# Kernel optimization log

Measured on AMD Instinct MI355X. Metric: run time of the kernel, lower is better.

## Reference

```python
import jax, jax.numpy as jnp
import numpy as np

N_NODES = 50000
N_EDGES = 800000
IN_DIM, HID_DIM, OUT_DIM = 128, 96, 40


def setup_inputs() -> dict:
    key = jax.random.key(0)
    ks = jax.random.split(key, 8)
    x = jax.random.normal(ks[0], (N_NODES, IN_DIM), dtype=jnp.float32)
    edge_src = jax.random.randint(ks[1], (N_EDGES,), 0, N_NODES, dtype=jnp.int32)
    edge_dst = jax.random.randint(ks[2], (N_EDGES,), 0, N_NODES, dtype=jnp.int32)
    edge_val = jax.random.uniform(ks[3], (N_EDGES,), dtype=jnp.float32)
    W1 = jax.random.normal(ks[4], (IN_DIM, HID_DIM), dtype=jnp.float32) * 0.05
    b1 = jax.random.normal(ks[5], (HID_DIM,), dtype=jnp.float32) * 0.05
    W2 = jax.random.normal(ks[6], (HID_DIM, OUT_DIM), dtype=jnp.float32) * 0.05
    b2 = jax.random.normal(ks[7], (OUT_DIM,), dtype=jnp.float32) * 0.05
    return {"x": x, "edge_val": edge_val, "W1": W1, "b1": b1,
            "W2": W2, "b2": b2, "edge_src": edge_src, "edge_dst": edge_dst}


def _spmm(edge_src, edge_dst, edge_val, dense, num_nodes):
    # out[i] = sum_{e: dst[e]==i} val[e] * dense[src[e]]  (COO sparse @ dense)
    msgs = edge_val[:, None] * dense[edge_src]  # [E, D]
    return jax.ops.segment_sum(msgs, edge_dst, num_segments=num_nodes)


def reference(x, edge_val, W1, b1, W2, b2, edge_src, edge_dst):
    n = x.shape[0]
    # GraphConv 1: support = x @ W1; out = A @ support + b1
    h = _spmm(edge_src, edge_dst, edge_val, x @ W1, n) + b1
    h = jax.nn.relu(h)  # dropout is identity in eval mode
    # GraphConv 2
    out = _spmm(edge_src, edge_dst, edge_val, h @ W2, n) + b2
    return jax.nn.log_softmax(out, axis=1)
```

## Files before the change

kernel.cpp:

```cpp
#include <hip/hip_runtime.h>
#include <hip/hip_fp16.h>
#include <math.h>

#define N_NODES 50000
#define N_EDGES 800000
#define IN_DIM 128
#define HID_DIM 96
#define OUT_DIM 40
#define CAP 48
#define NB_G1 782
#define NB_CHUNK8 391
#define SLICE 6250

typedef __attribute__((ext_vector_type(8))) unsigned short ushort8_t;
typedef __attribute__((ext_vector_type(8))) short short8_t;
typedef __attribute__((ext_vector_type(4))) float floatx4_t;

static __device__ __forceinline__ unsigned short f2bf(float f) {
    unsigned int u = __float_as_uint(f);
    u += 0x7FFFu + ((u >> 16) & 1u);
    return (unsigned short)(u >> 16);
}
static __device__ __forceinline__ float bf2f(unsigned short h) {
    return __uint_as_float(((unsigned int)h) << 16);
}
static __device__ __forceinline__ float rec2w(unsigned int r) {
    return __half2float(__ushort_as_half((unsigned short)(r >> 16)));
}

__global__ __launch_bounds__(256) void gemm1_fill_kernel(
    const float* __restrict__ x, const float* __restrict__ W1,
    unsigned short* __restrict__ supb,
    const int* __restrict__ esrc, const int* __restrict__ edst,
    const float* __restrict__ eval, int* __restrict__ cnt,
    unsigned int* __restrict__ recs, int n) {
    const int b = blockIdx.x;
    const int t = threadIdx.x;

    if (b >= NB_G1) {
        const int i = b - NB_G1;
        const int slice = b & 7;
        const int chunk = i >> 3;
        const int e0 = chunk * 2048 + t * 8;
        if (e0 < N_EDGES) {
            const int4 d4a = *(const int4*)(edst + e0);
            const int4 d4b = *(const int4*)(edst + e0 + 4);
            const int lo = slice * SLICE;
            int dv[8] = {d4a.x, d4a.y, d4a.z, d4a.w,
                         d4b.x, d4b.y, d4b.z, d4b.w};
            #pragma unroll
            for (int j = 0; j < 8; ++j) {
                int d = dv[j];
                if ((unsigned)(d - lo) < (unsigned)SLICE) {
                    int e = e0 + j;
                    int pos = atomicAdd(&cnt[d], 1);
                    if (pos < CAP) {
                        unsigned int rec = (unsigned int)esrc[e] |
                            ((unsigned int)__half_as_ushort(__float2half(eval[e])) << 16);
                        recs[(size_t)d * CAP + pos] = rec;
                    }
                }
            }
        }
        return;
    }

    __shared__ unsigned short sB[24 * 64 * 8];
    for (int i = t; i < IN_DIM * HID_DIM; i += 256) {
        int k = i / HID_DIM, nn = i - k * HID_DIM;
        int c = k >> 5, q = (k >> 3) & 3, j = k & 7;
        int g = nn >> 4, l16 = nn & 15;
        sB[(((c * 6 + g) * 64) + q * 16 + l16) * 8 + j] = f2bf(W1[i]);
    }
    __syncthreads();

    const int wave = t >> 6, lane = t & 63;
    const int m = lane & 15, q = lane >> 4;
    const int r0 = b * 64 + wave * 16;
    const int row = r0 + m;
    const bool rok = row < n;

    floatx4_t acc[6];
    #pragma unroll
    for (int g = 0; g < 6; ++g) acc[g] = (floatx4_t){0.f, 0.f, 0.f, 0.f};

    #pragma unroll
    for (int c = 0; c < 4; ++c) {
        float4 a0 = make_float4(0.f, 0.f, 0.f, 0.f), a1 = a0;
        if (rok) {
            const float4* xp = (const float4*)(x + (size_t)row * IN_DIM + c * 32 + q * 8);
            a0 = xp[0];
            a1 = xp[1];
        }
        short8_t af;
        af[0] = (short)f2bf(a0.x); af[1] = (short)f2bf(a0.y);
        af[2] = (short)f2bf(a0.z); af[3] = (short)f2bf(a0.w);
        af[4] = (short)f2bf(a1.x); af[5] = (short)f2bf(a1.y);
        af[6] = (short)f2bf(a1.z); af[7] = (short)f2bf(a1.w);
        #pragma unroll
        for (int g = 0; g < 6; ++g) {
            short8_t bf = *(const short8_t*)&sB[(((c * 6 + g) * 64) + lane) * 8];
            acc[g] = __builtin_amdgcn_mfma_f32_16x16x32_bf16(af, bf, acc[g], 0, 0, 0);
        }
    }

    #pragma unroll
    for (int r = 0; r < 4; ++r) {
        int ro = r0 + q * 4 + r;
        if (ro < n) {
            #pragma unroll
            for (int g = 0; g < 6; ++g)
                supb[(size_t)ro * HID_DIM + g * 16 + m] = f2bf(acc[g][r]);
        }
    }
}

__global__ __launch_bounds__(256) void gather1_gemm2_kernel(
    const unsigned short* __restrict__ supb, const unsigned int* __restrict__ recs,
    const int* __restrict__ cnt, const float* __restrict__ b1,
    const float* __restrict__ W2, unsigned short* __restrict__ yb) {
    __shared__ float sH[21][HID_DIM + 4];
    __shared__ float sW2[HID_DIM * OUT_DIM];
    __shared__ unsigned int sRec[21][52];
    const int t = threadIdx.x;
    const int dst0 = blockIdx.x * 21;
    const int g = t / 12, l = t % 12;
    const int dst = dst0 + g;
    const bool active = (t < 252) && (dst < N_NODES);

    for (int i = t; i < HID_DIM * OUT_DIM / 4; i += 256)
        ((float4*)sW2)[i] = ((const float4*)W2)[i];

    for (int i = t; i < 21 * 12; i += 256) {
        int gg = i / 12, qq = i % 12;
        int dd = dst0 + gg;
        if (dd < N_NODES)
            ((uint4*)&sRec[gg][0])[qq] = ((const uint4*)(recs + (size_t)dd * CAP))[qq];
    }
    __syncthreads();

    if (active) {
        int deg = cnt[dst];
        deg = deg < CAP ? deg : CAP;
        float acc[8] = {};
        const int c8 = l;
        const unsigned int* rg = &sRec[g][0];
        int p = 0;
        for (; p + 4 <= deg; p += 4) {
            unsigned int r0 = rg[p + 0], r1 = rg[p + 1];
            unsigned int r2 = rg[p + 2], r3 = rg[p + 3];
            ushort8_t v0 = ((const ushort8_t*)(supb + (size_t)(r0 & 0xFFFFu) * HID_DIM))[c8];
            ushort8_t v1 = ((const ushort8_t*)(supb + (size_t)(r1 & 0xFFFFu) * HID_DIM))[c8];
            ushort8_t v2 = ((const ushort8_t*)(supb + (size_t)(r2 & 0xFFFFu) * HID_DIM))[c8];
            ushort8_t v3 = ((const ushort8_t*)(supb + (size_t)(r3 & 0xFFFFu) * HID_DIM))[c8];
            float w0 = rec2w(r0), w1 = rec2w(r1), w2 = rec2w(r2), w3 = rec2w(r3);
            #pragma unroll
            for (int j = 0; j < 8; ++j) {
                acc[j] += w0 * bf2f(v0[j]);
                acc[j] += w1 * bf2f(v1[j]);
                acc[j] += w2 * bf2f(v2[j]);
                acc[j] += w3 * bf2f(v3[j]);
            }
        }
        for (; p < deg; ++p) {
            unsigned int r = rg[p];
            ushort8_t sv = ((const ushort8_t*)(supb + (size_t)(r & 0xFFFFu) * HID_DIM))[c8];
            float v = rec2w(r);
            #pragma unroll
            for (int j = 0; j < 8; ++j) acc[j] += v * bf2f(sv[j]);
        }
        float4 r0, r1;
        r0.x = fmaxf(acc[0] + b1[c8 * 8 + 0], 0.f);
        r0.y = fmaxf(acc[1] + b1[c8 * 8 + 1], 0.f);
        r0.z = fmaxf(acc[2] + b1[c8 * 8 + 2], 0.f);
        r0.w = fmaxf(acc[3] + b1[c8 * 8 + 3], 0.f);
        r1.x = fmaxf(acc[4] + b1[c8 * 8 + 4], 0.f);
        r1.y = fmaxf(acc[5] + b1[c8 * 8 + 5], 0.f);
        r1.z = fmaxf(acc[6] + b1[c8 * 8 + 6], 0.f);
        r1.w = fmaxf(acc[7] + b1[c8 * 8 + 7], 0.f);
        float4* hp = (float4*)&sH[g][c8 * 8];
        hp[0] = r0;
        hp[1] = r1;
    }
    __syncthreads();

    for (int idx = t; idx < 21 * OUT_DIM; idx += 256) {
        int d = idx / OUT_DIM, c = idx % OUT_DIM;
        int dd = dst0 + d;
        if (dd >= N_NODES) continue;
        const float4* hr = (const float4*)&sH[d][0];
        float s = 0.f;
        #pragma unroll
        for (int k4 = 0; k4 < HID_DIM / 4; ++k4) {
            float4 hv = hr[k4];
            s += hv.x * sW2[(k4 * 4 + 0) * OUT_DIM + c]
               + hv.y * sW2[(k4 * 4 + 1) * OUT_DIM + c]
               + hv.z * sW2[(k4 * 4 + 2) * OUT_DIM + c]
               + hv.w * sW2[(k4 * 4 + 3) * OUT_DIM + c];
        }
        yb[(size_t)dd * OUT_DIM + c] = f2bf(s);
    }
}

__global__ __launch_bounds__(256) void gather2_lsm_kernel(
    const unsigned short* __restrict__ yb, const unsigned int* __restrict__ recs,
    const int* __restrict__ cnt, const float* __restrict__ b2,
    float* __restrict__ out) {
    __shared__ unsigned int sRec[50][52];
    __shared__ float part[256];
    __shared__ float smax[50];
    __shared__ float ssum[50];
    const int t = threadIdx.x;
    const int g = t / 5;
    const int c8 = t % 5;
    int dst = blockIdx.x * 50 + g;
    bool active = (t < 250) && (dst < N_NODES);

    for (int i = t; i < 50 * 12; i += 256) {
        int gg = i / 12, qq = i % 12;
        int dd = blockIdx.x * 50 + gg;
        if (dd < N_NODES)
            ((uint4*)&sRec[gg][0])[qq] = ((const uint4*)(recs + (size_t)dd * CAP))[qq];
    }
    __syncthreads();

    float acc[8] = {};
    if (active) {
        int deg = cnt[dst];
        deg = deg < CAP ? deg : CAP;
        const unsigned int* rg = &sRec[g][0];
        int p = 0;
        for (; p + 4 <= deg; p += 4) {
            unsigned int r0 = rg[p + 0], r1 = rg[p + 1];
            unsigned int r2 = rg[p + 2], r3 = rg[p + 3];
            ushort8_t v0 = ((const ushort8_t*)(yb + (size_t)(r0 & 0xFFFFu) * OUT_DIM))[c8];
            ushort8_t v1 = ((const ushort8_t*)(yb + (size_t)(r1 & 0xFFFFu) * OUT_DIM))[c8];
            ushort8_t v2 = ((const ushort8_t*)(yb + (size_t)(r2 & 0xFFFFu) * OUT_DIM))[c8];
            ushort8_t v3 = ((const ushort8_t*)(yb + (size_t)(r3 & 0xFFFFu) * OUT_DIM))[c8];
            float w0 = rec2w(r0), w1 = rec2w(r1), w2 = rec2w(r2), w3 = rec2w(r3);
            #pragma unroll
            for (int j = 0; j < 8; ++j) {
                acc[j] += w0 * bf2f(v0[j]);
                acc[j] += w1 * bf2f(v1[j]);
                acc[j] += w2 * bf2f(v2[j]);
                acc[j] += w3 * bf2f(v3[j]);
            }
        }
        for (; p < deg; ++p) {
            unsigned int r = rg[p];
            ushort8_t sv = ((const ushort8_t*)(yb + (size_t)(r & 0xFFFFu) * OUT_DIM))[c8];
            float v = rec2w(r);
            #pragma unroll
            for (int j = 0; j < 8; ++j) acc[j] += v * bf2f(sv[j]);
        }
        #pragma unroll
        for (int j = 0; j < 8; ++j) acc[j] += b2[c8 * 8 + j];
    }
    float lmax = -INFINITY;
    #pragma unroll
    for (int j = 0; j < 8; ++j) lmax = fmaxf(lmax, acc[j]);
    part[t] = active ? lmax : -INFINITY;
    __syncthreads();
    if (t < 50) {
        float m = part[t * 5];
        #pragma unroll
        for (int i = 1; i < 5; ++i) m = fmaxf(m, part[t * 5 + i]);
        smax[t] = m;
    }
    __syncthreads();
    float m = active ? smax[g] : 0.f;
    float lsum = 0.f;
    #pragma unroll
    for (int j = 0; j < 8; ++j) lsum += expf(acc[j] - m);
    part[t] = active ? lsum : 0.f;
    __syncthreads();
    if (t < 50) {
        float s = 0.f;
        #pragma unroll
        for (int i = 0; i < 5; ++i) s += part[t * 5 + i];
        ssum[t] = logf(s);
    }
    __syncthreads();
    if (active) {
        float ls = ssum[g];
        float* op = out + (size_t)dst * OUT_DIM + c8 * 8;
        ((float4*)op)[0] = make_float4(acc[0] - m - ls, acc[1] - m - ls,
                                       acc[2] - m - ls, acc[3] - m - ls);
        ((float4*)op)[1] = make_float4(acc[4] - m - ls, acc[5] - m - ls,
                                       acc[6] - m - ls, acc[7] - m - ls);
    }
}

extern "C" void kernel_launch(void* const* d_in, const int* in_sizes, int n_in,
                              void* d_out, int out_size, void* d_ws, size_t ws_size,
                              hipStream_t stream) {
    const float* x        = (const float*)d_in[0];
    const float* edge_val = (const float*)d_in[1];
    const float* W1       = (const float*)d_in[2];
    const float* b1       = (const float*)d_in[3];
    const float* W2       = (const float*)d_in[4];
    const float* b2       = (const float*)d_in[5];
    const int*   esrc     = (const int*)d_in[6];
    const int*   edst     = (const int*)d_in[7];
    float* out = (float*)d_out;

    int*   cnt  = (int*)d_ws;
    unsigned int* recs = (unsigned int*)(cnt + 50048);
    unsigned short* supb = (unsigned short*)(recs + (size_t)N_NODES * CAP);
    unsigned short* yb   = supb + (size_t)N_NODES * HID_DIM;

    hipMemsetAsync(cnt, 0, N_NODES * sizeof(int), stream);
    gemm1_fill_kernel<<<NB_G1 + NB_CHUNK8 * 8, 256, 0, stream>>>(
        x, W1, supb, esrc, edst, edge_val, cnt, recs, N_NODES);
    gather1_gemm2_kernel<<<(N_NODES + 20) / 21, 256, 0, stream>>>(
        supb, recs, cnt, b1, W2, yb);
    gather2_lsm_kernel<<<(N_NODES + 49) / 50, 256, 0, stream>>>(
        yb, recs, cnt, b2, out);
}
```

Measured before the change: 183.3 us.

## Fuse three GCN stages into one cooperative kernel with grid syncs

Replaces the three separate launches (gemm1+bucket fill, gather1+gemm2, gather2+log_softmax) with a single persistent cooperative kernel of 1016 blocks that uses grid-wide syncs between phases. Blocks loop over work items in phases that previously had more blocks than the grid. The aim is to remove kernel launch gaps and tail effects between stages. In exchange it adds grid-sync cost, a fixed grid that may underfill some phases, and a fallback to the old path if the cooperative launch fails.

```diff
diff --git a/kernel.cpp b/kernel.cpp
--- a/kernel.cpp
+++ b/kernel.cpp
@@ -1,5 +1,6 @@
 #include <hip/hip_runtime.h>
 #include <hip/hip_fp16.h>
+#include <hip/hip_cooperative_groups.h>
 #include <math.h>
 
 #define N_NODES 50000
@@ -9,12 +10,18 @@
 #define OUT_DIM 40
 #define CAP 48
 #define NB_G1 782
-#define NB_CHUNK8 391
+#define GRID 1016
+#define FILL_PB 127
+#define NCHUNK 391
 #define SLICE 6250
+#define NGRP_B 2381
+#define NGRP_C 1000
 
 typedef __attribute__((ext_vector_type(8))) unsigned short ushort8_t;
 typedef __attribute__((ext_vector_type(8))) short short8_t;
 typedef __attribute__((ext_vector_type(4))) float floatx4_t;
+
+namespace cg = cooperative_groups;
 
 static __device__ __forceinline__ unsigned short f2bf(float f) {
     unsigned int u = __float_as_uint(f);
@@ -26,6 +33,276 @@
 }
 static __device__ __forceinline__ float rec2w(unsigned int r) {
     return __half2float(__ushort_as_half((unsigned short)(r >> 16)));
+}
+
+__global__ __launch_bounds__(256, 4) void fused_kernel(
+    const float* __restrict__ x, const float* __restrict__ W1,
+    unsigned short* __restrict__ supb,
+    const int* __restrict__ esrc, const int* __restrict__ edst,
+    const float* __restrict__ eval, int* __restrict__ cnt,
+    unsigned int* __restrict__ recs,
+    const float* __restrict__ b1, const float* __restrict__ W2,
+    const float* __restrict__ b2,
+    unsigned short* __restrict__ yb, float* __restrict__ out) {
+    __shared__ __align__(16) unsigned char smem[28160];
+    const int bid = blockIdx.x;
+    const int t = threadIdx.x;
+    cg::grid_group gg_grid = cg::this_grid();
+
+    if (bid < NB_G1) {
+        unsigned short* sB = (unsigned short*)smem;
+        for (int i = t; i < IN_DIM * HID_DIM; i += 256) {
+            int k = i / HID_DIM, nn = i - k * HID_DIM;
+            int c = k >> 5, q2 = (k >> 3) & 3, j = k & 7;
+            int g2 = nn >> 4, l16 = nn & 15;
+            sB[(((c * 6 + g2) * 64) + q2 * 16 + l16) * 8 + j] = f2bf(W1[i]);
+        }
+        __syncthreads();
+
+        const int wave = t >> 6, lane = t & 63;
+        const int m = lane & 15, q = lane >> 4;
+        const int r0 = bid * 64 + wave * 16;
+        const int row = r0 + m;
+        const bool rok = row < N_NODES;
+
+        floatx4_t acc[6];
+        #pragma unroll
+        for (int g = 0; g < 6; ++g) acc[g] = (floatx4_t){0.f, 0.f, 0.f, 0.f};
+
+        #pragma unroll
+        for (int c = 0; c < 4; ++c) {
+            float4 a0 = make_float4(0.f, 0.f, 0.f, 0.f), a1 = a0;
+            if (rok) {
+                const float4* xp = (const float4*)(x + (size_t)row * IN_DIM + c * 32 + q * 8);
+                a0 = xp[0];
+                a1 = xp[1];
+            }
+            short8_t af;
+            af[0] = (short)f2bf(a0.x); af[1] = (short)f2bf(a0.y);
+            af[2] = (short)f2bf(a0.z); af[3] = (short)f2bf(a0.w);
+            af[4] = (short)f2bf(a1.x); af[5] = (short)f2bf(a1.y);
+            af[6] = (short)f2bf(a1.z); af[7] = (short)f2bf(a1.w);
+            #pragma unroll
+            for (int g = 0; g < 6; ++g) {
+                short8_t bf = *(const short8_t*)&sB[(((c * 6 + g) * 64) + lane) * 8];
+                acc[g] = __builtin_amdgcn_mfma_f32_16x16x32_bf16(af, bf, acc[g], 0, 0, 0);
+            }
+        }
+
+        #pragma unroll
+        for (int r = 0; r < 4; ++r) {
+            int ro = r0 + q * 4 + r;
+            if (ro < N_NODES) {
+                #pragma unroll
+                for (int g = 0; g < 6; ++g)
+                    supb[(size_t)ro * HID_DIM + g * 16 + m] = f2bf(acc[g][r]);
+            }
+        }
+    }
+
+    {
+        const int slice = bid & 7;
+        const int lo = slice * SLICE;
+        for (int chunk = bid >> 3; chunk < NCHUNK; chunk += FILL_PB) {
+            const int e0 = chunk * 2048 + t * 8;
+            if (e0 < N_EDGES) {
+                const int4 d4a = *(const int4*)(edst + e0);
+                const int4 d4b = *(const int4*)(edst + e0 + 4);
+                int dv[8] = {d4a.x, d4a.y, d4a.z, d4a.w,
+                             d4b.x, d4b.y, d4b.z, d4b.w};
+                #pragma unroll
+                for (int j = 0; j < 8; ++j) {
+                    int d = dv[j];
+                    if ((unsigned)(d - lo) < (unsigned)SLICE) {
+                        int e = e0 + j;
+                        int pos = atomicAdd(&cnt[d], 1);
+                        if (pos < CAP) {
+                            unsigned int rec = (unsigned int)esrc[e] |
+                                ((unsigned int)__half_as_ushort(__float2half(eval[e])) << 16);
+                            recs[(size_t)d * CAP + pos] = rec;
+                        }
+                    }
+                }
+            }
+        }
+    }
+
+    __threadfence();
+    gg_grid.sync();
+
+    {
+        float* sW2 = (float*)smem;
+        float* sH = (float*)(smem + 15360);
+        unsigned int* sRec = (unsigned int*)(smem + 23760);
+
+        for (int i = t; i < HID_DIM * OUT_DIM / 4; i += 256)
+            ((float4*)sW2)[i] = ((const float4*)W2)[i];
+
+        for (int grp = bid; grp < NGRP_B; grp += GRID) {
+            __syncthreads();
+            const int dst0 = grp * 21;
+            for (int i = t; i < 21 * 12; i += 256) {
+                int g2 = i / 12, qq = i % 12;
+                int dd = dst0 + g2;
+                if (dd < N_NODES)
+                    ((uint4*)&sRec[g2 * 52])[qq] = ((const uint4*)(recs + (size_t)dd * CAP))[qq];
+            }
+            __syncthreads();
+
+            const int g = t / 12, l = t % 12;
+            const int dst = dst0 + g;
+            const bool active = (t < 252) && (dst < N_NODES);
+            if (active) {
+                int deg = cnt[dst];
+                deg = deg < CAP ? deg : CAP;
+                float acc[8] = {};
+                const int c8 = l;
+                const unsigned int* rg = &sRec[g * 52];
+                int p = 0;
+                for (; p + 4 <= deg; p += 4) {
+                    unsigned int r0 = rg[p + 0], r1 = rg[p + 1];
+                    unsigned int r2 = rg[p + 2], r3 = rg[p + 3];
+                    ushort8_t v0 = ((const ushort8_t*)(supb + (size_t)(r0 & 0xFFFFu) * HID_DIM))[c8];
+                    ushort8_t v1 = ((const ushort8_t*)(supb + (size_t)(r1 & 0xFFFFu) * HID_DIM))[c8];
+                    ushort8_t v2 = ((const ushort8_t*)(supb + (size_t)(r2 & 0xFFFFu) * HID_DIM))[c8];
+                    ushort8_t v3 = ((const ushort8_t*)(supb + (size_t)(r3 & 0xFFFFu) * HID_DIM))[c8];
+                    float w0 = rec2w(r0), w1 = rec2w(r1), w2 = rec2w(r2), w3 = rec2w(r3);
+                    #pragma unroll
+                    for (int j = 0; j < 8; ++j) {
+                        acc[j] += w0 * bf2f(v0[j]);
+                        acc[j] += w1 * bf2f(v1[j]);
+                        acc[j] += w2 * bf2f(v2[j]);
+                        acc[j] += w3 * bf2f(v3[j]);
+                    }
+                }
+                for (; p < deg; ++p) {
+                    unsigned int r = rg[p];
+                    ushort8_t sv = ((const ushort8_t*)(supb + (size_t)(r & 0xFFFFu) * HID_DIM))[c8];
+                    float v = rec2w(r);
+                    #pragma unroll
+                    for (int j = 0; j < 8; ++j) acc[j] += v * bf2f(sv[j]);
+                }
+                float4 r0v, r1v;
+                r0v.x = fmaxf(acc[0] + b1[c8 * 8 + 0], 0.f);
+                r0v.y = fmaxf(acc[1] + b1[c8 * 8 + 1], 0.f);
+                r0v.z = fmaxf(acc[2] + b1[c8 * 8 + 2], 0.f);
+                r0v.w = fmaxf(acc[3] + b1[c8 * 8 + 3], 0.f);
+                r1v.x = fmaxf(acc[4] + b1[c8 * 8 + 4], 0.f);
+                r1v.y = fmaxf(acc[5] + b1[c8 * 8 + 5], 0.f);
+                r1v.z = fmaxf(acc[6] + b1[c8 * 8 + 6], 0.f);
+                r1v.w = fmaxf(acc[7] + b1[c8 * 8 + 7], 0.f);
+                float4* hp = (float4*)&sH[g * 100 + c8 * 8];
+                hp[0] = r0v;
+                hp[1] = r1v;
+            }
+            __syncthreads();
+
+            for (int idx = t; idx < 21 * OUT_DIM; idx += 256) {
+                int d = idx / OUT_DIM, c = idx % OUT_DIM;
+                int dd = dst0 + d;
+                if (dd >= N_NODES) continue;
+                const float4* hr = (const float4*)&sH[d * 100];
+                float s = 0.f;
+                #pragma unroll
+                for (int k4 = 0; k4 < HID_DIM / 4; ++k4) {
+                    float4 hv = hr[k4];
+                    s += hv.x * sW2[(k4 * 4 + 0) * OUT_DIM + c]
+                       + hv.y * sW2[(k4 * 4 + 1) * OUT_DIM + c]
+                       + hv.z * sW2[(k4 * 4 + 2) * OUT_DIM + c]
+                       + hv.w * sW2[(k4 * 4 + 3) * OUT_DIM + c];
+                }
+                yb[(size_t)dd * OUT_DIM + c] = f2bf(s);
+            }
+        }
+    }
+
+    __threadfence();
+    gg_grid.sync();
+
+    if (bid < NGRP_C) {
+        unsigned int* sRec = (unsigned int*)smem;
+        float* part = (float*)(smem + 10400);
+        float* smax = (float*)(smem + 11424);
+        float* ssum = (float*)(smem + 11624);
+        const int g = t / 5;
+        const int c8 = t % 5;
+        const int dst = bid * 50 + g;
+        const bool active = (t < 250) && (dst < N_NODES);
+
+        for (int i = t; i < 50 * 12; i += 256) {
+            int g2 = i / 12, qq = i % 12;
+            int dd = bid * 50 + g2;
+            if (dd < N_NODES)
+                ((uint4*)&sRec[g2 * 52])[qq] = ((const uint4*)(recs + (size_t)dd * CAP))[qq];
+        }
+        __syncthreads();
+
+        float acc[8] = {};
+        if (active) {
+            int deg = cnt[dst];
+            deg = deg < CAP ? deg : CAP;
+            const unsigned int* rg = &sRec[g * 52];
+            int p = 0;
+            for (; p + 4 <= deg; p += 4) {
+                unsigned int r0 = rg[p + 0], r1 = rg[p + 1];
+                unsigned int r2 = rg[p + 2], r3 = rg[p + 3];
+                ushort8_t v0 = ((const ushort8_t*)(yb + (size_t)(r0 & 0xFFFFu) * OUT_DIM))[c8];
+                ushort8_t v1 = ((const ushort8_t*)(yb + (size_t)(r1 & 0xFFFFu) * OUT_DIM))[c8];
+                ushort8_t v2 = ((const ushort8_t*)(yb + (size_t)(r2 & 0xFFFFu) * OUT_DIM))[c8];
+                ushort8_t v3 = ((const ushort8_t*)(yb + (size_t)(r3 & 0xFFFFu) * OUT_DIM))[c8];
+                float w0 = rec2w(r0), w1 = rec2w(r1), w2 = rec2w(r2), w3 = rec2w(r3);
+                #pragma unroll
+                for (int j = 0; j < 8; ++j) {
+                    acc[j] += w0 * bf2f(v0[j]);
+                    acc[j] += w1 * bf2f(v1[j]);
+                    acc[j] += w2 * bf2f(v2[j]);
+                    acc[j] += w3 * bf2f(v3[j]);
+                }
+            }
+            for (; p < deg; ++p) {
+                unsigned int r = rg[p];
+                ushort8_t sv = ((const ushort8_t*)(yb + (size_t)(r & 0xFFFFu) * OUT_DIM))[c8];
+                float v = rec2w(r);
+                #pragma unroll
+                for (int j = 0; j < 8; ++j) acc[j] += v * bf2f(sv[j]);
+            }
+            #pragma unroll
+            for (int j = 0; j < 8; ++j) acc[j] += b2[c8 * 8 + j];
+        }
+        float lmax = -INFINITY;
+        #pragma unroll
+        for (int j = 0; j < 8; ++j) lmax = fmaxf(lmax, acc[j]);
+        part[t] = active ? lmax : -INFINITY;
+        __syncthreads();
+        if (t < 50) {
+            float m = part[t * 5];
+            #pragma unroll
+            for (int i = 1; i < 5; ++i) m = fmaxf(m, part[t * 5 + i]);
+            smax[t] = m;
+        }
+        __syncthreads();
+        float m = active ? smax[g] : 0.f;
+        float lsum = 0.f;
+        #pragma unroll
+        for (int j = 0; j < 8; ++j) lsum += expf(acc[j] - m);
+        part[t] = active ? lsum : 0.f;
+        __syncthreads();
+        if (t < 50) {
+            float s = 0.f;
+            #pragma unroll
+            for (int i = 0; i < 5; ++i) s += part[t * 5 + i];
+            ssum[t] = logf(s);
+        }
+        __syncthreads();
+        if (active) {
+            float ls = ssum[g];
+            float* op = out + (size_t)dst * OUT_DIM + c8 * 8;
+            ((float4*)op)[0] = make_float4(acc[0] - m - ls, acc[1] - m - ls,
+                                           acc[2] - m - ls, acc[3] - m - ls);
+            ((float4*)op)[1] = make_float4(acc[4] - m - ls, acc[5] - m - ls,
+                                           acc[6] - m - ls, acc[7] - m - ls);
+        }
+    }
 }
 
 __global__ __launch_bounds__(256) void gemm1_fill_kernel(
@@ -310,10 +587,18 @@
     unsigned short* yb   = supb + (size_t)N_NODES * HID_DIM;
 
     hipMemsetAsync(cnt, 0, N_NODES * sizeof(int), stream);
-    gemm1_fill_kernel<<<NB_G1 + NB_CHUNK8 * 8, 256, 0, stream>>>(
-        x, W1, supb, esrc, edst, edge_val, cnt, recs, N_NODES);
-    gather1_gemm2_kernel<<<(N_NODES + 20) / 21, 256, 0, stream>>>(
-        supb, recs, cnt, b1, W2, yb);
-    gather2_lsm_kernel<<<(N_NODES + 49) / 50, 256, 0, stream>>>(
-        yb, recs, cnt, b2, out);
-}
+
+    void* kargs[] = {(void*)&x, (void*)&W1, (void*)&supb, (void*)&esrc,
+                     (void*)&edst, (void*)&edge_val, (void*)&cnt, (void*)&recs,
+                     (void*)&b1, (void*)&W2, (void*)&b2, (void*)&yb, (void*)&out};
+    hipError_t err = hipLaunchCooperativeKernel(
+        (const void*)fused_kernel, dim3(GRID), dim3(256), kargs, 0, stream);
+    if (err != hipSuccess) {
+        gemm1_fill_kernel<<<NB_G1 + NCHUNK * 8, 256, 0, stream>>>(
+            x, W1, supb, esrc, edst, edge_val, cnt, recs, N_NODES);
+        gather1_gemm2_kernel<<<(N_NODES + 20) / 21, 256, 0, stream>>>(
+            supb, recs, cnt, b1, W2, yb);
+        gather2_lsm_kernel<<<(N_NODES + 49) / 50, 256, 0, stream>>>(
+            yb, recs, cnt, b2, out);
+    }
+}
```

New measurement: 655.9 us. 3.58x slower.
